# Kernel tuning notes

Hardware: AMD Instinct MI355X
Metric: run time of the kernel (lower is better)

## Reference

```python
import jax, jax.numpy as jnp
import numpy as np

B, T, D, H, L, C = 512, 512, 128, 16, 5, 2


def setup_inputs() -> dict:
    key = jax.random.key(0)
    ks = jax.random.split(key, 12)
    x = jax.random.normal(ks[0], (B, T, D), dtype=jnp.float32)
    # pack_padded_sequence requires descending lengths; force max length == T
    lengths = jnp.sort(jax.random.randint(ks[1], (B,), 1, T + 1))[::-1]
    lengths = lengths.at[0].set(T)
    s = 0.25  # ~ 1/sqrt(H) init scale
    W_ih0 = jax.random.normal(ks[2], (3 * H, D), dtype=jnp.float32) * s
    W_ihr = jax.random.normal(ks[3], (L - 1, 3 * H, H), dtype=jnp.float32) * s
    W_hh = jax.random.normal(ks[4], (L, 3 * H, H), dtype=jnp.float32) * s
    b_ih = jax.random.normal(ks[5], (L, 3 * H), dtype=jnp.float32) * s
    b_hh = jax.random.normal(ks[6], (L, 3 * H), dtype=jnp.float32) * s
    W_fc = jax.random.normal(ks[7], (C, H), dtype=jnp.float32) * s
    b_fc = jax.random.normal(ks[8], (C,), dtype=jnp.float32) * s
    return {"x": x, "lengths": lengths, "W_ih0": W_ih0, "W_ihr": W_ihr,
            "W_hh": W_hh, "b_ih": b_ih, "b_hh": b_hh, "W_fc": W_fc, "b_fc": b_fc}


def _gru_layer(seq, Wih, Whh, bih, bhh):
    # seq: [T, B, Din] -> outputs [T, B, H]. PyTorch GRU gate math.
    xg = jnp.einsum('tbd,gd->tbg', seq, Wih) + bih  # precompute input projections

    def step(h, xg_t):
        hg = h @ Whh.T + bhh
        xr, xz, xn = jnp.split(xg_t, 3, axis=-1)
        hr, hz, hn = jnp.split(hg, 3, axis=-1)
        r = jax.nn.sigmoid(xr + hr)
        z = jax.nn.sigmoid(xz + hz)
        n = jnp.tanh(xn + r * hn)
        h_new = (1.0 - z) * n + z * h
        return h_new, h_new

    h0 = jnp.zeros((seq.shape[1], Whh.shape[1]), seq.dtype)
    _, ys = jax.lax.scan(step, h0, xg)
    return ys


def reference(x, lengths, W_ih0, W_ihr, W_hh, b_ih, b_hh, W_fc, b_fc):
    seq = jnp.transpose(x, (1, 0, 2))  # [T, B, D]
    seq = _gru_layer(seq, W_ih0, W_hh[0], b_ih[0], b_hh[0])
    for l in range(L - 1):  # dropout(0.5) between layers: eval mode (identity)
        seq = _gru_layer(seq, W_ihr[l], W_hh[l + 1], b_ih[l + 1], b_hh[l + 1])
    last = seq[T - 1]  # [B, H] == padded output[:, -1, :]
    # pad_packed_sequence zero-pads: rows with length < T are zero at t = T-1
    last = jnp.where((lengths == T)[:, None], last, 0.0)
    return last @ W_fc.T + b_fc
```

## Files before the change

kernel.cpp:

```cpp
#include <hip/hip_runtime.h>


constexpr int kB = 512, kT = 512, kD = 128, kH = 16, kL = 5, kC = 2, kG = 48;
constexpr int kChunk = 16, kNC = kT / kChunk, kThreads = 320;
constexpr int kPhases = kNC + 2 * (kL - 1);
constexpr int kYW = 64;
constexpr float kLog2e = 1.4426950408889634f;

typedef unsigned uint2v __attribute__((ext_vector_type(2)));

__device__ __forceinline__ float rl(float v, int lane) {
    return __int_as_float(__builtin_amdgcn_readlane(__float_as_int(v), lane));
}

__device__ __forceinline__ float fexp2(float x) {
#if __has_builtin(__builtin_amdgcn_exp2f)
    return __builtin_amdgcn_exp2f(x);
#else
    return exp2f(x);
#endif
}

#if __has_builtin(__builtin_amdgcn_permlane32_swap) && __has_builtin(__builtin_amdgcn_permlane16_swap)
__device__ __forceinline__ float sel_other(uint2v r, float self) {
    unsigned s = __float_as_uint(self);
    return __uint_as_float((r[0] == s) ? r[1] : r[0]);
}
__device__ __forceinline__ float xor32(float v) {
    uint2v r = __builtin_amdgcn_permlane32_swap(__float_as_uint(v), __float_as_uint(v), false, false);
    return sel_other(r, v);
}
__device__ __forceinline__ float xor16(float v) {
    uint2v r = __builtin_amdgcn_permlane16_swap(__float_as_uint(v), __float_as_uint(v), false, false);
    return sel_other(r, v);
}
#else
__device__ __forceinline__ float bperm_xor(float v, int xmask) {
    int lane = threadIdx.x & 63;
    return __int_as_float(__builtin_amdgcn_ds_bpermute((lane ^ xmask) * 4, __float_as_int(v)));
}
__device__ __forceinline__ float xor32(float v) { return bperm_xor(v, 32); }
__device__ __forceinline__ float xor16(float v) { return bperm_xor(v, 16); }
#endif

__device__ __forceinline__ float gru_step(float h, float xg,
                                          const float (&wreg)[kH], float bh) {
    float a0 = bh, a1 = 0.f, a2 = 0.f, a3 = 0.f;
    #pragma unroll
    for (int k = 0; k < 4; ++k) {
        a0 = fmaf(rl(h, k),      wreg[k],      a0);
        a1 = fmaf(rl(h, k + 4),  wreg[k + 4],  a1);
        a2 = fmaf(rl(h, k + 8),  wreg[k + 8],  a2);
        a3 = fmaf(rl(h, k + 12), wreg[k + 12], a3);
    }
    float xnb = xor32(xg);
    float hg = (a0 + a1) + (a2 + a3);
    float hnb = xor32(hg);
    float s = xg + hg;
    float sig = __builtin_amdgcn_rcpf(1.0f + fexp2(-s));
    float zb = xor16(sig);
    float narg = fmaf(sig, hnb, xnb);
    float nv = fmaf(-2.0f, __builtin_amdgcn_rcpf(fexp2(narg) + 1.0f), 1.0f);
    return fmaf(zb, h - nv, nv);
}

template<bool SCAN, int PREP, bool WY>
__device__ __forceinline__ float phase_body(
    float h, float (&xgr)[kChunk], const float* __restrict__ gsrc,
    const float (*__restrict__ yprev)[kYW], float (*__restrict__ yout)[kYW],
    const float (&wreg)[kH], float bh, const float (&wih)[kH], float bi,
    int lane)
{
    float4 ra0, ra1, ra2, ra3;
    if (PREP == 2) {
        const float4* y4 = (const float4*)&yprev[0][0];
        ra0 = y4[0]; ra1 = y4[1]; ra2 = y4[2]; ra3 = y4[3];
    }
    #pragma unroll
    for (int tt = 0; tt < kChunk; ++tt) {
        float4 rb0 = ra0, rb1 = ra1, rb2 = ra2, rb3 = ra3;
        if (PREP == 2 && tt + 1 < kChunk) {
            const float4* y4 = (const float4*)&yprev[tt + 1][0];
            rb0 = y4[0]; rb1 = y4[1]; rb2 = y4[2]; rb3 = y4[3];
        }
        if (SCAN) {
            h = gru_step(h, xgr[tt], wreg, bh);
            if (WY) yout[tt][lane] = h;
        }
        if (PREP == 1) {
            xgr[tt] = gsrc[(size_t)tt * kG];
        } else if (PREP == 2) {
            float p0 = bi, p1 = 0.f, p2 = 0.f, p3 = 0.f;
            p0 = fmaf(ra0.x, wih[0],  p0); p0 = fmaf(ra0.y, wih[1],  p0);
            p0 = fmaf(ra0.z, wih[2],  p0); p0 = fmaf(ra0.w, wih[3],  p0);
            p1 = fmaf(ra1.x, wih[4],  p1); p1 = fmaf(ra1.y, wih[5],  p1);
            p1 = fmaf(ra1.z, wih[6],  p1); p1 = fmaf(ra1.w, wih[7],  p1);
            p2 = fmaf(ra2.x, wih[8],  p2); p2 = fmaf(ra2.y, wih[9],  p2);
            p2 = fmaf(ra2.z, wih[10], p2); p2 = fmaf(ra2.w, wih[11], p2);
            p3 = fmaf(ra3.x, wih[12], p3); p3 = fmaf(ra3.y, wih[13], p3);
            p3 = fmaf(ra3.z, wih[14], p3); p3 = fmaf(ra3.w, wih[15], p3);
            xgr[tt] = (p0 + p1) + (p2 + p3);
            ra0 = rb0; ra1 = rb1; ra2 = rb2; ra3 = rb3;
        }
    }
    return h;
}

extern "C" __global__ void __launch_bounds__(256, 1)
proj0(const float* __restrict__ x, const int* __restrict__ len,
      const float* __restrict__ Wih0, const float* __restrict__ bih,
      float* __restrict__ xg0, int qmax)
{
    const int blk = blockIdx.x;
    const int b = blk >> 4, s = blk & 15;
    if (b >= qmax || len[b] != kT) return;
    const int tid = threadIdx.x;
    #pragma unroll
    for (int i = 0; i < 6; ++i) {
        int item = tid + 256 * i;
        int t = item / kG, g = item - t * kG;
        const float4* xr = (const float4*)(x + ((size_t)b * kT + s * 32 + t) * kD);
        const float4* wr = (const float4*)(Wih0 + (size_t)g * kD);
        float a0 = 0.f, a1 = 0.f, a2 = 0.f, a3 = 0.f;
        #pragma unroll 8
        for (int k = 0; k < kD / 4; ++k) {
            float4 xv = xr[k], wv = wr[k];
            a0 = fmaf(xv.x, wv.x, a0);
            a1 = fmaf(xv.y, wv.y, a1);
            a2 = fmaf(xv.z, wv.z, a2);
            a3 = fmaf(xv.w, wv.w, a3);
        }
        float scg = (g < 32) ? kLog2e : 2.0f * kLog2e;
        xg0[((size_t)b * kT + s * 32 + t) * kG + g] =
            scg * (bih[g] + ((a0 + a1) + (a2 + a3)));
    }
}

__device__ void proj_chunk_wave0(const float* __restrict__ x,
                                 const float* __restrict__ Wih0,
                                 const float* __restrict__ bih,
                                 int b, int c, int lane, float (*__restrict__ XW0)[kG])
{
    for (int i = 0; i < kChunk * kG / 64; ++i) {
        int item = lane + 64 * i;
        int t = item / kG, g = item - t * kG;
        const float4* xr = (const float4*)(x + ((size_t)b * kT + c * kChunk + t) * kD);
        const float4* wr = (const float4*)(Wih0 + (size_t)g * kD);
        float a0 = 0.f, a1 = 0.f, a2 = 0.f, a3 = 0.f;
        #pragma unroll 8
        for (int k = 0; k < kD / 4; ++k) {
            float4 xv = xr[k], wv = wr[k];
            a0 = fmaf(xv.x, wv.x, a0);
            a1 = fmaf(xv.y, wv.y, a1);
            a2 = fmaf(xv.z, wv.z, a2);
            a3 = fmaf(xv.w, wv.w, a3);
        }
        float scg = (g < 32) ? kLog2e : 2.0f * kLog2e;
        XW0[t][g] = scg * (bih[g] + ((a0 + a1) + (a2 + a3)));
    }
}

__device__ __forceinline__ void barrier_lgkm() {
    asm volatile("s_waitcnt lgkmcnt(0)" ::: "memory");
    __builtin_amdgcn_s_barrier();
}

extern "C" __global__ void __launch_bounds__(kThreads, 1)
gru_pipe4(const float* __restrict__ x, const int* __restrict__ len,
          const float* __restrict__ Wih0, const float* __restrict__ Wihr,
          const float* __restrict__ Whh, const float* __restrict__ bih,
          const float* __restrict__ bhh, const float* __restrict__ Wfc,
          const float* __restrict__ bfc, const float* __restrict__ xg0,
          float* __restrict__ out, int qmax)
{
    const int b = blockIdx.x;
    const int tid = threadIdx.x;

    if (len[b] != kT) {
        if (tid < kC) out[b * kC + tid] = bfc[tid];
        return;
    }

    __shared__ float Yr[kL - 1][2][kChunk][kYW];
    __shared__ float XW0[kChunk][kG];
    __shared__ float hfin[kH];

    const int wid = tid >> 6, lane = tid & 63;
    const int g = (lane < kG) ? lane : (kG - 1);
    const bool fast = (b < qmax);
    const float* xgb = xg0 + (size_t)b * kT * kG + g;
    const float sc = (g < 32) ? kLog2e : 2.0f * kLog2e;

    float wreg[kH], wih[kH];
    float bh, bi = 0.f, h = 0.f;
    {
        const float* wrow = Whh + (size_t)(wid * kG + g) * kH;
        #pragma unroll
        for (int k = 0; k < kH; ++k) wreg[k] = wrow[k] * sc;
        bh = bhh[wid * kG + g] * sc;
        if (wid > 0) {
            const float* wr2 = Wihr + (size_t)((wid - 1) * kG + g) * kH;
            #pragma unroll
            for (int k = 0; k < kH; ++k) wih[k] = wr2[k] * sc;
            bi = bih[wid * kG + g] * sc;
        } else {
            #pragma unroll
            for (int k = 0; k < kH; ++k) wih[k] = 0.f;
        }
    }

    float xgr[kChunk];
    if (wid == 0) {
        if (fast) {
            #pragma unroll
            for (int tt = 0; tt < kChunk; ++tt) xgr[tt] = xgb[(size_t)tt * kG];
        } else {
            proj_chunk_wave0(x, Wih0, bih, b, 0, lane, XW0);
            asm volatile("s_waitcnt lgkmcnt(0)" ::: "memory");
            #pragma unroll
            for (int tt = 0; tt < kChunk; ++tt) xgr[tt] = XW0[tt][g];
        }
    }

    for (int p = 0; p < kPhases; ++p) {
        const int c = p - 2 * wid;
        const bool sc_ = (c >= 0 && c < kNC);
        const bool pr = (c + 1 >= 0 && c + 1 < kNC);
        if (wid == 0) {
            float (*yo)[kYW] = Yr[0][c & 1];
            if (fast) {
                const float* gsrc = xgb + (size_t)(c + 1) * kChunk * kG;
                if (sc_ && pr)
                    h = phase_body<true, 1, true>(h, xgr, gsrc, nullptr, yo, wreg, bh, wih, bi, lane);
                else if (sc_)
                    h = phase_body<true, 0, true>(h, xgr, nullptr, nullptr, yo, wreg, bh, wih, bi, lane);
            } else {
                if (sc_)
                    h = phase_body<true, 0, true>(h, xgr, nullptr, nullptr, yo, wreg, bh, wih, bi, lane);
                if (pr) {
                    proj_chunk_wave0(x, Wih0, bih, b, c + 1, lane, XW0);
                    asm volatile("s_waitcnt lgkmcnt(0)" ::: "memory");
                    #pragma unroll
                    for (int tt = 0; tt < kChunk; ++tt) xgr[tt] = XW0[tt][g];
                }
            }
        } else {
            const float (*yp)[kYW] = Yr[wid - 1][(c + 1) & 1];
            float (*yo)[kYW] = Yr[(wid < kL - 1) ? wid : 0][c & 1];
            if (wid < kL - 1) {
                if (sc_ && pr)
                    h = phase_body<true, 2, true>(h, xgr, nullptr, yp, yo, wreg, bh, wih, bi, lane);
                else if (sc_)
                    h = phase_body<true, 0, true>(h, xgr, nullptr, yp, yo, wreg, bh, wih, bi, lane);
                else if (pr)
                    h = phase_body<false, 2, false>(h, xgr, nullptr, yp, yo, wreg, bh, wih, bi, lane);
            } else {
                if (sc_ && pr)
                    h = phase_body<true, 2, false>(h, xgr, nullptr, yp, yo, wreg, bh, wih, bi, lane);
                else if (sc_)
                    h = phase_body<true, 0, false>(h, xgr, nullptr, yp, yo, wreg, bh, wih, bi, lane);
                else if (pr)
                    h = phase_body<false, 2, false>(h, xgr, nullptr, yp, yo, wreg, bh, wih, bi, lane);
            }
        }
        barrier_lgkm();
    }

    if (wid == kL - 1 && lane < kH) hfin[lane] = h;
    __syncthreads();

    if (tid < kC) {
        float acc = bfc[tid];
        #pragma unroll
        for (int j = 0; j < kH; ++j)
            acc = fmaf(hfin[j], Wfc[tid * kH + j], acc);
        out[b * kC + tid] = acc;
    }
}

extern "C" void kernel_launch(void* const* d_in, const int* in_sizes, int n_in,
                              void* d_out, int out_size, void* d_ws, size_t ws_size,
                              hipStream_t stream) {
    const float* x    = (const float*)d_in[0];
    const int*   len  = (const int*)d_in[1];
    const float* Wih0 = (const float*)d_in[2];
    const float* Wihr = (const float*)d_in[3];
    const float* Whh  = (const float*)d_in[4];
    const float* bih  = (const float*)d_in[5];
    const float* bhh  = (const float*)d_in[6];
    const float* Wfc  = (const float*)d_in[7];
    const float* bfc  = (const float*)d_in[8];
    float* outp = (float*)d_out;
    float* xg0  = (float*)d_ws;

    size_t per_row = (size_t)kT * kG * sizeof(float);
    int qmax = (int)((ws_size / per_row) < (size_t)kB ? (ws_size / per_row) : (size_t)kB);

    hipLaunchKernelGGL(proj0, dim3(kB * 16), dim3(256), 0, stream,
                       x, len, Wih0, bih, xg0, qmax);
    hipLaunchKernelGGL(gru_pipe4, dim3(kB), dim3(kThreads), 0, stream,
                       x, len, Wih0, Wihr, Whh, bih, bhh, Wfc, bfc, xg0, outp, qmax);
}
```

Baseline: 181.1 us.

## Fold last GRU layer into wave 0, shrinking block to four waves

The fifth wave, which ran layer 4, is removed. Wave 0 now interleaves the layer-0 scan with the layer-4 scan, which trails by 8 phases, so the block drops from 320 to 256 threads. The aim is to fill wave 0's idle slots in the serial recurrence with independent work and to cut the wave count per block. The cost is more registers and a longer dependency-interleaved body in wave 0, which could lengthen the critical path per phase.

```diff
diff --git a/kernel.cpp b/kernel.cpp
--- a/kernel.cpp
+++ b/kernel.cpp
@@ -2,8 +2,8 @@
 
 
 constexpr int kB = 512, kT = 512, kD = 128, kH = 16, kL = 5, kC = 2, kG = 48;
-constexpr int kChunk = 16, kNC = kT / kChunk, kThreads = 320;
-constexpr int kPhases = kNC + 2 * (kL - 1);
+constexpr int kChunk = 16, kNC = kT / kChunk, kThreads = 256;
+constexpr int kPhases = kNC + 8;
 constexpr int kYW = 64;
 constexpr float kLog2e = 1.4426950408889634f;
 
@@ -64,9 +64,9 @@
     return fmaf(zb, h - nv, nv);
 }
 
-template<bool SCAN, int PREP, bool WY>
+template<bool SCAN, int PREP>
 __device__ __forceinline__ float phase_body(
-    float h, float (&xgr)[kChunk], const float* __restrict__ gsrc,
+    float h, float (&xgr)[kChunk],
     const float (*__restrict__ yprev)[kYW], float (*__restrict__ yout)[kYW],
     const float (&wreg)[kH], float bh, const float (&wih)[kH], float bi,
     int lane)
@@ -85,11 +85,9 @@
         }
         if (SCAN) {
             h = gru_step(h, xgr[tt], wreg, bh);
-            if (WY) yout[tt][lane] = h;
-        }
-        if (PREP == 1) {
-            xgr[tt] = gsrc[(size_t)tt * kG];
-        } else if (PREP == 2) {
+            yout[tt][lane] = h;
+        }
+        if (PREP == 2) {
             float p0 = bi, p1 = 0.f, p2 = 0.f, p3 = 0.f;
             p0 = fmaf(ra0.x, wih[0],  p0); p0 = fmaf(ra0.y, wih[1],  p0);
             p0 = fmaf(ra0.z, wih[2],  p0); p0 = fmaf(ra0.w, wih[3],  p0);
@@ -104,6 +102,52 @@
         }
     }
     return h;
+}
+
+template<bool SA, bool PA, bool SB, bool PB>
+__device__ __forceinline__ void w0_phase(
+    float& hA, float& hB, float (&xgrA)[kChunk], float (&xgrB)[kChunk],
+    const float* __restrict__ gsrcA,
+    const float (*__restrict__ y3)[kYW], float (*__restrict__ y0)[kYW],
+    const float (&wA)[kH], float bhA, const float (&wB)[kH], float bhB,
+    const float (&wihB)[kH], float biB, int lane)
+{
+    float4 ra0, ra1, ra2, ra3;
+    if (PB) {
+        const float4* y4 = (const float4*)&y3[0][0];
+        ra0 = y4[0]; ra1 = y4[1]; ra2 = y4[2]; ra3 = y4[3];
+    }
+    #pragma unroll
+    for (int tt = 0; tt < kChunk; ++tt) {
+        float4 rb0 = ra0, rb1 = ra1, rb2 = ra2, rb3 = ra3;
+        if (PB && tt + 1 < kChunk) {
+            const float4* y4 = (const float4*)&y3[tt + 1][0];
+            rb0 = y4[0]; rb1 = y4[1]; rb2 = y4[2]; rb3 = y4[3];
+        }
+        if (SA) {
+            hA = gru_step(hA, xgrA[tt], wA, bhA);
+            y0[tt][lane] = hA;
+        }
+        if (SB) {
+            hB = gru_step(hB, xgrB[tt], wB, bhB);
+        }
+        if (PA) {
+            xgrA[tt] = gsrcA[(size_t)tt * kG];
+        }
+        if (PB) {
+            float p0 = biB, p1 = 0.f, p2 = 0.f, p3 = 0.f;
+            p0 = fmaf(ra0.x, wihB[0],  p0); p0 = fmaf(ra0.y, wihB[1],  p0);
+            p0 = fmaf(ra0.z, wihB[2],  p0); p0 = fmaf(ra0.w, wihB[3],  p0);
+            p1 = fmaf(ra1.x, wihB[4],  p1); p1 = fmaf(ra1.y, wihB[5],  p1);
+            p1 = fmaf(ra1.z, wihB[6],  p1); p1 = fmaf(ra1.w, wihB[7],  p1);
+            p2 = fmaf(ra2.x, wihB[8],  p2); p2 = fmaf(ra2.y, wihB[9],  p2);
+            p2 = fmaf(ra2.z, wihB[10], p2); p2 = fmaf(ra2.w, wihB[11], p2);
+            p3 = fmaf(ra3.x, wihB[12], p3); p3 = fmaf(ra3.y, wihB[13], p3);
+            p3 = fmaf(ra3.z, wihB[14], p3); p3 = fmaf(ra3.w, wihB[15], p3);
+            xgrB[tt] = (p0 + p1) + (p2 + p3);
+            ra0 = rb0; ra1 = rb1; ra2 = rb2; ra3 = rb3;
+        }
+    }
 }
 
 extern "C" __global__ void __launch_bounds__(256, 1)
@@ -166,7 +210,7 @@
 }
 
 extern "C" __global__ void __launch_bounds__(kThreads, 1)
-gru_pipe4(const float* __restrict__ x, const int* __restrict__ len,
+gru_pipe5(const float* __restrict__ x, const int* __restrict__ len,
           const float* __restrict__ Wih0, const float* __restrict__ Wihr,
           const float* __restrict__ Whh, const float* __restrict__ bih,
           const float* __restrict__ bhh, const float* __restrict__ Wfc,
@@ -191,25 +235,36 @@
     const float* xgb = xg0 + (size_t)b * kT * kG + g;
     const float sc = (g < 32) ? kLog2e : 2.0f * kLog2e;
 
-    float wreg[kH], wih[kH];
-    float bh, bi = 0.f, h = 0.f;
-    {
+    float wreg[kH], wih[kH], wregB[kH], wihB[kH];
+    float bh = 0.f, bi = 0.f, bhB = 0.f, biB = 0.f, h = 0.f, hB = 0.f;
+    if (wid == 0) {
+        const float* wrow = Whh + (size_t)g * kH;
+        const float* wrowB = Whh + (size_t)(4 * kG + g) * kH;
+        const float* wihrB = Wihr + (size_t)(3 * kG + g) * kH;
+        #pragma unroll
+        for (int k = 0; k < kH; ++k) {
+            wreg[k]  = wrow[k] * sc;
+            wregB[k] = wrowB[k] * sc;
+            wihB[k]  = wihrB[k] * sc;
+            wih[k] = 0.f;
+        }
+        bh  = bhh[g] * sc;
+        bhB = bhh[4 * kG + g] * sc;
+        biB = bih[4 * kG + g] * sc;
+    } else {
         const float* wrow = Whh + (size_t)(wid * kG + g) * kH;
+        const float* wr2  = Wihr + (size_t)((wid - 1) * kG + g) * kH;
         #pragma unroll
-        for (int k = 0; k < kH; ++k) wreg[k] = wrow[k] * sc;
+        for (int k = 0; k < kH; ++k) {
+            wreg[k] = wrow[k] * sc;
+            wih[k]  = wr2[k] * sc;
+            wregB[k] = 0.f; wihB[k] = 0.f;
+        }
         bh = bhh[wid * kG + g] * sc;
-        if (wid > 0) {
-            const float* wr2 = Wihr + (size_t)((wid - 1) * kG + g) * kH;
-            #pragma unroll
-            for (int k = 0; k < kH; ++k) wih[k] = wr2[k] * sc;
-            bi = bih[wid * kG + g] * sc;
-        } else {
-            #pragma unroll
-            for (int k = 0; k < kH; ++k) wih[k] = 0.f;
-        }
-    }
-
-    float xgr[kChunk];
+        bi = bih[wid * kG + g] * sc;
+    }
+
+    float xgr[kChunk], xgrB[kChunk];
     if (wid == 0) {
         if (fast) {
             #pragma unroll
@@ -223,50 +278,59 @@
     }
 
     for (int p = 0; p < kPhases; ++p) {
-        const int c = p - 2 * wid;
-        const bool sc_ = (c >= 0 && c < kNC);
-        const bool pr = (c + 1 >= 0 && c + 1 < kNC);
         if (wid == 0) {
-            float (*yo)[kYW] = Yr[0][c & 1];
+            const int cA = p, cB = p - 8;
+            const float* gsrcA = xgb + (size_t)(cA + 1) * kChunk * kG;
+            const float (*y3)[kYW] = Yr[3][(cB + 1) & 1];
+            float (*y0)[kYW] = Yr[0][cA & 1];
             if (fast) {
-                const float* gsrc = xgb + (size_t)(c + 1) * kChunk * kG;
-                if (sc_ && pr)
-                    h = phase_body<true, 1, true>(h, xgr, gsrc, nullptr, yo, wreg, bh, wih, bi, lane);
-                else if (sc_)
-                    h = phase_body<true, 0, true>(h, xgr, nullptr, nullptr, yo, wreg, bh, wih, bi, lane);
+                if (p < 7)
+                    w0_phase<1,1,0,0>(h, hB, xgr, xgrB, gsrcA, y3, y0, wreg, bh, wregB, bhB, wihB, biB, lane);
+                else if (p == 7)
+                    w0_phase<1,1,0,1>(h, hB, xgr, xgrB, gsrcA, y3, y0, wreg, bh, wregB, bhB, wihB, biB, lane);
+                else if (p < 31)
+                    w0_phase<1,1,1,1>(h, hB, xgr, xgrB, gsrcA, y3, y0, wreg, bh, wregB, bhB, wihB, biB, lane);
+                else if (p == 31)
+                    w0_phase<1,0,1,1>(h, hB, xgr, xgrB, gsrcA, y3, y0, wreg, bh, wregB, bhB, wihB, biB, lane);
+                else if (p < 39)
+                    w0_phase<0,0,1,1>(h, hB, xgr, xgrB, gsrcA, y3, y0, wreg, bh, wregB, bhB, wihB, biB, lane);
+                else
+                    w0_phase<0,0,1,0>(h, hB, xgr, xgrB, gsrcA, y3, y0, wreg, bh, wregB, bhB, wihB, biB, lane);
             } else {
-                if (sc_)
-                    h = phase_body<true, 0, true>(h, xgr, nullptr, nullptr, yo, wreg, bh, wih, bi, lane);
-                if (pr) {
-                    proj_chunk_wave0(x, Wih0, bih, b, c + 1, lane, XW0);
+                if (p < 7)
+                    w0_phase<1,0,0,0>(h, hB, xgr, xgrB, gsrcA, y3, y0, wreg, bh, wregB, bhB, wihB, biB, lane);
+                else if (p == 7)
+                    w0_phase<1,0,0,1>(h, hB, xgr, xgrB, gsrcA, y3, y0, wreg, bh, wregB, bhB, wihB, biB, lane);
+                else if (p < 32)
+                    w0_phase<1,0,1,1>(h, hB, xgr, xgrB, gsrcA, y3, y0, wreg, bh, wregB, bhB, wihB, biB, lane);
+                else if (p < 39)
+                    w0_phase<0,0,1,1>(h, hB, xgr, xgrB, gsrcA, y3, y0, wreg, bh, wregB, bhB, wihB, biB, lane);
+                else
+                    w0_phase<0,0,1,0>(h, hB, xgr, xgrB, gsrcA, y3, y0, wreg, bh, wregB, bhB, wihB, biB, lane);
+                if (p + 1 < kNC) {
+                    proj_chunk_wave0(x, Wih0, bih, b, p + 1, lane, XW0);
                     asm volatile("s_waitcnt lgkmcnt(0)" ::: "memory");
                     #pragma unroll
                     for (int tt = 0; tt < kChunk; ++tt) xgr[tt] = XW0[tt][g];
                 }
             }
         } else {
+            const int c = p - 2 * wid;
+            const bool sc_ = (c >= 0 && c < kNC);
+            const bool pr = (c + 1 >= 0 && c + 1 < kNC);
             const float (*yp)[kYW] = Yr[wid - 1][(c + 1) & 1];
-            float (*yo)[kYW] = Yr[(wid < kL - 1) ? wid : 0][c & 1];
-            if (wid < kL - 1) {
-                if (sc_ && pr)
-                    h = phase_body<true, 2, true>(h, xgr, nullptr, yp, yo, wreg, bh, wih, bi, lane);
-                else if (sc_)
-                    h = phase_body<true, 0, true>(h, xgr, nullptr, yp, yo, wreg, bh, wih, bi, lane);
-                else if (pr)
-                    h = phase_body<false, 2, false>(h, xgr, nullptr, yp, yo, wreg, bh, wih, bi, lane);
-            } else {
-                if (sc_ && pr)
-                    h = phase_body<true, 2, false>(h, xgr, nullptr, yp, yo, wreg, bh, wih, bi, lane);
-                else if (sc_)
-                    h = phase_body<true, 0, false>(h, xgr, nullptr, yp, yo, wreg, bh, wih, bi, lane);
-                else if (pr)
-                    h = phase_body<false, 2, false>(h, xgr, nullptr, yp, yo, wreg, bh, wih, bi, lane);
-            }
+            float (*yo)[kYW] = Yr[wid][c & 1];
+            if (sc_ && pr)
+                h = phase_body<true, 2>(h, xgr, yp, yo, wreg, bh, wih, bi, lane);
+            else if (sc_)
+                h = phase_body<true, 0>(h, xgr, yp, yo, wreg, bh, wih, bi, lane);
+            else if (pr)
+                h = phase_body<false, 2>(h, xgr, yp, yo, wreg, bh, wih, bi, lane);
         }
         barrier_lgkm();
     }
 
-    if (wid == kL - 1 && lane < kH) hfin[lane] = h;
+    if (wid == 0 && lane < kH) hfin[lane] = hB;
     __syncthreads();
 
     if (tid < kC) {
@@ -298,6 +362,6 @@
 
     hipLaunchKernelGGL(proj0, dim3(kB * 16), dim3(256), 0, stream,
                        x, len, Wih0, bih, xg0, qmax);
-    hipLaunchKernelGGL(gru_pipe4, dim3(kB), dim3(kThreads), 0, stream,
+    hipLaunchKernelGGL(gru_pipe5, dim3(kB), dim3(kThreads), 0, stream,
                        x, len, Wih0, Wihr, Whh, bih, bhh, Wfc, bfc, xg0, outp, qmax);
 }
```

Measured after the change: 197.2 us. 8.9% more time.
